# Performance work log

Hardware: AMD Instinct MI355X
Metric: run time of the kernel (lower is better)

## Reference

```python
import jax, jax.numpy as jnp
import numpy as np

B, T, NV, DEG, E = 64, 256, 20000, 8, 128
NSEG, NBUCKET = NV * DEG, 288
F_DIST, F_DIR, F_TT, HID = 50, 50, 50, 100
FEED = 2 * E + F_DIST + F_DIR  # 356


def setup_inputs() -> dict:
    key = jax.random.key(0)
    ks = jax.random.split(key, 32)
    s = 1.0 / np.sqrt(E)
    return {
        "xs_padded": jax.random.randint(ks[0], (B, T), 0, NV),
        "lengths": jax.random.randint(ks[1], (B,), 8, T + 1),
        "xs_actions": jax.random.randint(ks[2], (B, T - 1), 0, DEG),
        "destinations": jax.random.randint(ks[3], (B,), 0, NV),
        "adj_list": jax.random.randint(ks[4], (NV, DEG), 0, NV),
        "seg_ids": jax.random.randint(ks[5], (NV, DEG), 0, NSEG),
        "start_time": 42,
        "locations": jax.random.normal(ks[6], (NV, 2)),
        "time_dist_seg": jax.random.uniform(ks[7], (NSEG, NBUCKET)) * 10.0,
        "emb": jax.random.normal(ks[8], (NV + 2, E)) * 0.01,
        "Wq": jax.random.normal(ks[9], (E, E)) * s,
        "Wk": jax.random.normal(ks[10], (E, E)) * s,
        "Wv": jax.random.normal(ks[11], (E, E)) * s,
        "Wo": jax.random.normal(ks[12], (E, E)) * s,
        "dist_W": jax.random.normal(ks[13], (1, F_DIST)),
        "dist_b": jnp.zeros((F_DIST,)),
        "dir_W": jax.random.normal(ks[14], (2, F_DIR)) * 0.7,
        "dir_b": jnp.zeros((F_DIR,)),
        "tt_W": jax.random.normal(ks[15], (1, F_TT)),
        "tt_b": jnp.zeros((F_TT,)),
        "ob_W1": jax.random.normal(ks[16], (F_TT, F_TT // 2)) * (1.0 / np.sqrt(F_TT)),
        "ob_b1": jnp.zeros((F_TT // 2,)),
        "ob_W2": jax.random.normal(ks[17], (F_TT // 2, 1)) * (1.0 / np.sqrt(F_TT // 2)),
        "ob_b2": jnp.zeros((1,)),
        "om_W1": jax.random.normal(ks[18], (FEED, HID)) * (1.0 / np.sqrt(FEED)),
        "om_b1": jnp.zeros((HID,)),
        "om_W2": jax.random.normal(ks[19], (HID, HID // 2)) * (1.0 / np.sqrt(HID)),
        "om_b2": jnp.zeros((HID // 2,)),
        "om_W3": jax.random.normal(ks[20], (HID // 2, 1)) * (1.0 / np.sqrt(HID // 2)),
        "om_b3": jnp.zeros((1,)),
    }


def reference(xs_padded, lengths, xs_actions, destinations, adj_list, seg_ids,
              start_time, locations, time_dist_seg, emb, Wq, Wk, Wv, Wo,
              dist_W, dist_b, dir_W, dir_b, tt_W, tt_b,
              ob_W1, ob_b1, ob_W2, ob_b2,
              om_W1, om_b1, om_W2, om_b2, om_W3, om_b3):
    # --- embeddings + causal/padding-masked self-attention (flash_att) ---
    x_e = emb[xs_padded]                                       # [B,T,E]
    q, k, v = x_e @ Wq, x_e @ Wk, x_e @ Wv
    scores = jnp.einsum('bqe,bke->bqk', q, k) / jnp.sqrt(jnp.float32(E))
    causal = jnp.triu(jnp.ones((T, T), bool), 1)
    pad = jnp.arange(T)[None, :] >= lengths[:, None]           # key padding [B,T]
    scores = jnp.where(causal[None] | pad[:, None, :], -1e9, scores)
    hidden = jnp.einsum('bqk,bke->bqe', jax.nn.softmax(scores, axis=-1), v) @ Wo

    # --- irregular neighbor gather: route_neighbors only filled for t < len-1 ---
    valid_t = jnp.arange(T)[None, :] < (lengths - 1)[:, None]  # [B,T]
    rn = jnp.where(valid_t[:, :, None], adj_list[xs_padded], 0)  # [B,T,DEG]

    # --- distance to destination feature ---
    dest_c = locations[destinations][:, None, None, :]         # [B,1,1,2]
    nbr_c = locations[rn]                                      # [B,T,DEG,2]
    dist = jnp.abs(nbr_c - dest_c).sum(-1, keepdims=True) * 100.0
    dist_f = dist @ dist_W + dist_b

    # --- direction (unit vector) feature ---
    vec = nbr_c - locations[xs_padded][:, :, None, :]
    unit = vec / (jnp.linalg.norm(vec, axis=-1, keepdims=True) + 1e-8)
    dir_f = unit @ dir_W + dir_b

    # --- travel-time lookup + masked whitening ---
    nmask = rn != 0
    tt = time_dist_seg[seg_ids[xs_padded], start_time]         # [B,T,DEG]
    mf = nmask.astype(tt.dtype)
    cnt = mf.sum()
    mean = (tt * mf).sum() / cnt
    var = (((tt - mean) ** 2) * mf).sum() / (cnt - 1.0)        # unbiased, like torch.std
    tt = (tt - mean) / (jnp.sqrt(var) + 1e-6)
    tt_f = (tt[..., None] @ tt_W + tt_b) * mf[..., None]

    # --- fuse and score neighbors ---
    hid_e = jnp.broadcast_to(hidden[:, :, None, :], (B, T, DEG, E))
    dest_e = jnp.broadcast_to(emb[destinations][:, None, None, :], (B, T, DEG, E))
    feed = jnp.concatenate([hid_e, dist_f, dir_f, dest_e], axis=-1)  # [B,T,DEG,356]

    ob = (jax.nn.relu(tt_f @ ob_W1 + ob_b1) @ ob_W2 + ob_b2).squeeze(-1)
    h1 = jax.nn.relu(feed @ om_W1 + om_b1)
    h2 = jax.nn.relu(h1 @ om_W2 + om_b2)
    logits = (h2 @ om_W3 + om_b3).squeeze(-1) + ob             # [B,T,DEG]

    # --- per-route mean cross-entropy over valid transitions, summed over batch ---
    logp = jax.nn.log_softmax(logits[:, :T - 1], axis=-1)
    nll = -jnp.take_along_axis(logp, xs_actions[..., None], axis=-1).squeeze(-1)
    vmask = (jnp.arange(T - 1)[None, :] < (lengths - 1)[:, None]).astype(nll.dtype)
    per = (nll * vmask).sum(1) / (lengths - 1).astype(nll.dtype)
    return per.sum()
```

## Files before the change

kernel.cpp:

```cpp
#include <hip/hip_runtime.h>
#include <math.h>

#define BB 64
#define TT 256
#define DEG 8
#define EE 128
#define NBUCKET 288
#define HID 100
#define H2 50

constexpr size_t OFF_STATS   = 0;
constexpr size_t OFF_CDIST   = 4;
constexpr size_t OFF_CDIRX   = 104;
constexpr size_t OFF_CDIRY   = 204;
constexpr size_t OFF_BASE    = 304;
constexpr size_t OFF_V25     = 404;
constexpr size_t OFF_C25     = 429;
constexpr size_t OFF_OBZ     = 454;
constexpr size_t OFF_DESTPRE = 456;
constexpr size_t OFF_WF      = 6856;
constexpr size_t OFF_WVF     = 19656;
constexpr size_t OFF_TT      = 32456;
constexpr size_t OFF_Q       = 163528;
constexpr size_t OFF_K       = OFF_Q + 16384 * 128;
constexpr size_t OFF_VP      = OFF_K + 16384 * 128;
constexpr size_t OFF_H1P     = OFF_VP + 16384 * 100;

__global__ void k_prevec(const float* dist_W, const float* dist_b,
                         const float* dir_W, const float* dir_b,
                         const float* tt_W, const float* tt_b,
                         const float* ob_W1, const float* ob_b1,
                         const float* ob_W2, const float* ob_b2,
                         const float* om_W1, const float* om_b1,
                         float* ws, float* out) {
    int j = threadIdx.x;
    if (j < 4) ws[OFF_STATS + j] = 0.f;
    if (j == 0) out[0] = 0.f;
    if (j < HID) {
        float cd = 0.f, cx = 0.f, cy = 0.f, bs = om_b1[j];
        for (int f = 0; f < 50; f++) {
            float w1d = om_W1[(128 + f) * HID + j];
            float w1r = om_W1[(178 + f) * HID + j];
            cd += dist_W[f] * w1d;
            bs += dist_b[f] * w1d + dir_b[f] * w1r;
            cx += dir_W[f] * w1r;
            cy += dir_W[50 + f] * w1r;
        }
        ws[OFF_CDIST + j] = cd; ws[OFF_CDIRX + j] = cx;
        ws[OFF_CDIRY + j] = cy; ws[OFF_BASE + j] = bs;
    }
    if (j < 25) {
        float v = 0.f, c = ob_b1[j];
        for (int i = 0; i < 50; i++) {
            v += tt_W[i] * ob_W1[i * 25 + j];
            c += tt_b[i] * ob_W1[i * 25 + j];
        }
        ws[OFF_V25 + j] = v; ws[OFF_C25 + j] = c;
    }
    if (j == 64) {
        float z = ob_b2[0];
        for (int i = 0; i < 25; i++) z += fmaxf(ob_b1[i], 0.f) * ob_W2[i];
        ws[OFF_OBZ] = z;
    }
}

__global__ void k_destpre(const int* destinations, const float* emb,
                          const float* om_W1, float* ws) {
    __shared__ float er[EE];
    int b = blockIdx.x;
    int d = destinations[b];
    er[threadIdx.x] = emb[(size_t)d * EE + threadIdx.x];
    __syncthreads();
    int m = threadIdx.x;
    if (m < HID) {
        float acc = 0.f;
        for (int i = 0; i < EE; i++) acc += er[i] * om_W1[(228 + i) * HID + m];
        ws[OFF_DESTPRE + b * HID + m] = acc;
    }
}

__global__ void k_wfused(const float* Wo, const float* om_W1, float* ws) {
    __shared__ float wr[EE];
    int i = blockIdx.x;
    wr[threadIdx.x] = Wo[i * EE + threadIdx.x];
    __syncthreads();
    int m = threadIdx.x;
    if (m < HID) {
        float acc = 0.f;
        for (int j = 0; j < EE; j++) acc += wr[j] * om_W1[j * HID + m];
        ws[OFF_WF + i * HID + m] = acc;
    }
}

__global__ void k_wvf(const float* Wv, float* ws) {
    __shared__ float wr[EE];
    int i = blockIdx.x;
    wr[threadIdx.x] = Wv[i * EE + threadIdx.x];
    __syncthreads();
    int m = threadIdx.x;
    if (m < HID) {
        float acc = 0.f;
        const float* WF = ws + OFF_WF;
        for (int j = 0; j < EE; j++) acc += wr[j] * WF[j * HID + m];
        ws[OFF_WVF + i * HID + m] = acc;
    }
}

__global__ void __launch_bounds__(256) k_qkv(const int* xs, const float* emb,
                      const float* Wq, const float* Wk, float* ws) {
    __shared__ float XT[EE][36];
    __shared__ int vids[32];
    int tid = threadIdx.x;
    int r0 = blockIdx.x * 32;
    if (tid < 32) vids[tid] = xs[r0 + tid];
    __syncthreads();
    for (int c = 0; c < 16; c++) {
        int idx = c * 256 + tid;
        int r = idx >> 7, i = idx & 127;
        XT[i][r] = emb[(size_t)vids[r] * EE + i];
    }
    __syncthreads();
    int cg = tid & 31, rg = tid >> 5;
    const float* Wmats[2] = {Wq, Wk};
    float* Omats[2] = {ws + OFF_Q, ws + OFF_K};
    for (int mtx = 0; mtx < 2; mtx++) {
        const float* W = Wmats[mtx];
        float acc[4][4];
        #pragma unroll
        for (int a = 0; a < 4; a++)
            #pragma unroll
            for (int bb = 0; bb < 4; bb++) acc[a][bb] = 0.f;
        #pragma unroll 4
        for (int i = 0; i < EE; i++) {
            float4 av = *(const float4*)&XT[i][rg << 2];
            float4 wv = *(const float4*)&W[i * EE + (cg << 2)];
            acc[0][0] += av.x * wv.x; acc[0][1] += av.x * wv.y; acc[0][2] += av.x * wv.z; acc[0][3] += av.x * wv.w;
            acc[1][0] += av.y * wv.x; acc[1][1] += av.y * wv.y; acc[1][2] += av.y * wv.z; acc[1][3] += av.y * wv.w;
            acc[2][0] += av.z * wv.x; acc[2][1] += av.z * wv.y; acc[2][2] += av.z * wv.z; acc[2][3] += av.z * wv.w;
            acc[3][0] += av.w * wv.x; acc[3][1] += av.w * wv.y; acc[3][2] += av.w * wv.z; acc[3][3] += av.w * wv.w;
        }
        float* O = Omats[mtx];
        #pragma unroll
        for (int j = 0; j < 4; j++)
            *(float4*)&O[(size_t)(r0 + (rg << 2) + j) * EE + (cg << 2)] =
                make_float4(acc[j][0], acc[j][1], acc[j][2], acc[j][3]);
    }
    if (cg < 25) {
        const float* W = ws + OFF_WVF;
        float acc[4][4];
        #pragma unroll
        for (int a = 0; a < 4; a++)
            #pragma unroll
            for (int bb = 0; bb < 4; bb++) acc[a][bb] = 0.f;
        #pragma unroll 4
        for (int i = 0; i < EE; i++) {
            float4 av = *(const float4*)&XT[i][rg << 2];
            float4 wv = *(const float4*)&W[i * HID + (cg << 2)];
            acc[0][0] += av.x * wv.x; acc[0][1] += av.x * wv.y; acc[0][2] += av.x * wv.z; acc[0][3] += av.x * wv.w;
            acc[1][0] += av.y * wv.x; acc[1][1] += av.y * wv.y; acc[1][2] += av.y * wv.z; acc[1][3] += av.y * wv.w;
            acc[2][0] += av.z * wv.x; acc[2][1] += av.z * wv.y; acc[2][2] += av.z * wv.z; acc[2][3] += av.z * wv.w;
            acc[3][0] += av.w * wv.x; acc[3][1] += av.w * wv.y; acc[3][2] += av.w * wv.z; acc[3][3] += av.w * wv.w;
        }
        float* VP = ws + OFF_VP;
        #pragma unroll
        for (int j = 0; j < 4; j++)
            *(float4*)&VP[(size_t)(r0 + (rg << 2) + j) * HID + (cg << 2)] =
                make_float4(acc[j][0], acc[j][1], acc[j][2], acc[j][3]);
    }
}

__global__ void __launch_bounds__(128) k_attn(const int* lengths, float* ws) {
    int blk = blockIdx.x;
    int b = blk >> 8;
    int t = blk & 255;
    int len = lengths[b];
    if (t >= len - 1) return;
    __shared__ float q4s[EE];
    __shared__ float sc[TT];
    __shared__ float redm[2], reds[2];
    int tid = threadIdx.x;
    const float* Q = ws + OFF_Q; const float* K = ws + OFF_K;
    const float* VP = ws + OFF_VP;
    q4s[tid] = Q[(size_t)blk * EE + tid];
    __syncthreads();
    const float4* q4 = (const float4*)q4s;
    float lmax = -1e30f;
    #pragma unroll
    for (int h = 0; h < 2; h++) {
        int kk = tid + h * 128;
        if (kk <= t) {
            const float4* kr = (const float4*)(K + ((size_t)(b * TT + kk)) * EE);
            float s = 0.f;
            #pragma unroll 8
            for (int i = 0; i < EE / 4; i++) {
                float4 a = q4[i]; float4 bb = kr[i];
                s += a.x * bb.x + a.y * bb.y + a.z * bb.z + a.w * bb.w;
            }
            s *= 0.08838834764831845f;
            sc[kk] = s;
            lmax = fmaxf(lmax, s);
        }
    }
    #pragma unroll
    for (int o = 32; o > 0; o >>= 1) lmax = fmaxf(lmax, __shfl_xor(lmax, o, 64));
    if ((tid & 63) == 0) redm[tid >> 6] = lmax;
    __syncthreads();
    float m = fmaxf(redm[0], redm[1]);
    float lsum = 0.f;
    #pragma unroll
    for (int h = 0; h < 2; h++) {
        int kk = tid + h * 128;
        if (kk <= t) { float p = __expf(sc[kk] - m); sc[kk] = p; lsum += p; }
    }
    #pragma unroll
    for (int o = 32; o > 0; o >>= 1) lsum += __shfl_xor(lsum, o, 64);
    if ((tid & 63) == 0) reds[tid >> 6] = lsum;
    __syncthreads();
    float inv = 1.f / (reds[0] + reds[1]);
    if (tid < HID) {
        size_t base = (size_t)(b * TT) * HID + tid;
        float a0 = 0.f, a1 = 0.f, a2 = 0.f, a3 = 0.f;
        int kk = 0;
        for (; kk + 4 <= t + 1; kk += 4) {
            a0 += sc[kk]     * VP[base + (size_t)kk * HID];
            a1 += sc[kk + 1] * VP[base + (size_t)(kk + 1) * HID];
            a2 += sc[kk + 2] * VP[base + (size_t)(kk + 2) * HID];
            a3 += sc[kk + 3] * VP[base + (size_t)(kk + 3) * HID];
        }
        for (; kk <= t; kk++) a0 += sc[kk] * VP[base + (size_t)kk * HID];
        float o = (a0 + a1 + a2 + a3) * inv;
        ws[OFF_H1P + (size_t)blk * HID + tid] =
            o + ws[OFF_BASE + tid] + ws[OFF_DESTPRE + b * HID + tid];
    }
}

__global__ void __launch_bounds__(256) k_stats(const int* xs, const int* lengths, const int* adj,
                        const int* seg, const int* stime, const float* tds,
                        float* ws) {
    int st = *stime;
    float lsum = 0.f, lsq = 0.f, lcnt = 0.f;
    int total = BB * TT * DEG;
    for (int idx = blockIdx.x * blockDim.x + threadIdx.x; idx < total;
         idx += gridDim.x * blockDim.x) {
        int d = idx & 7;
        int bt = idx >> 3;
        int t = bt & 255;
        int b = bt >> 8;
        int len = lengths[b];
        if (t >= len - 1) continue;
        int v = xs[bt];
        int sg = seg[v * DEG + d];
        float tt = tds[(size_t)sg * NBUCKET + st];
        ws[OFF_TT + idx] = tt;
        int a = adj[v * DEG + d];
        if (a != 0) { lsum += tt; lsq += tt * tt; lcnt += 1.f; }
    }
    __shared__ float rs[256], rq[256], rc[256];
    int tid = threadIdx.x;
    rs[tid] = lsum; rq[tid] = lsq; rc[tid] = lcnt;
    __syncthreads();
    for (int s = 128; s > 0; s >>= 1) {
        if (tid < s) { rs[tid] += rs[tid + s]; rq[tid] += rq[tid + s]; rc[tid] += rc[tid + s]; }
        __syncthreads();
    }
    if (tid == 0) {
        atomicAdd(&ws[OFF_STATS + 0], rs[0]);
        atomicAdd(&ws[OFF_STATS + 1], rq[0]);
        atomicAdd(&ws[OFF_STATS + 2], rc[0]);
    }
}

__global__ void __launch_bounds__(256) k_final(
    const int* xs, const int* lengths, const int* xs_actions, const int* destinations,
    const int* adj, const float* locations,
    const float* om_W2, const float* om_b2, const float* om_W3, const float* om_b3,
    const float* ob_W2, const float* ob_b2,
    const float* ws, float* out)
{
    __shared__ float W2T[H2][104];
    __shared__ float h1s[4][DEG][104];
    __shared__ float nlls[4];
    int tid = threadIdx.x;
    for (int idx = tid; idx < HID * H2; idx += 256) {
        int mm = idx / H2, n = idx - mm * H2;
        W2T[n][mm] = om_W2[idx];
    }
    if (tid < 4) nlls[tid] = 0.f;
    int w = tid >> 6, lane = tid & 63;
    int pi = blockIdx.x * 4 + w;
    int b = pi / (TT - 1), t = pi - b * (TT - 1);
    int len = lengths[b];
    bool valid = (t < len - 1);
    int bt = b * TT + t;
    int r = lane >> 3, li = lane & 7;
    __syncthreads();
    float distv = 0.f, uxv = 0.f, uyv = 0.f, obv = 0.f;
    if (valid) {
        float sum = ws[OFF_STATS], sq = ws[OFF_STATS + 1], cnt = ws[OFF_STATS + 2];
        float mean = sum / cnt;
        float var = (sq - cnt * mean * mean) / (cnt - 1.f);
        float sdinv = 1.f / (sqrtf(var) + 1e-6f);
        if (lane < 8) {
            int v = xs[bt];
            int a = adj[v * DEG + lane];
            float nbx = locations[2 * a], nby = locations[2 * a + 1];
            int dst = destinations[b];
            float dxl = locations[2 * dst], dyl = locations[2 * dst + 1];
            float cxl = locations[2 * v], cyl = locations[2 * v + 1];
            distv = (fabsf(nbx - dxl) + fabsf(nby - dyl)) * 100.f;
            float vx = nbx - cxl, vy = nby - cyl;
            float nrm = sqrtf(vx * vx + vy * vy) + 1e-8f;
            uxv = vx / nrm; uyv = vy / nrm;
            float ttn = (ws[OFF_TT + (size_t)bt * 8 + lane] - mean) * sdinv;
            float obp = 0.f;
            for (int j = 0; j < 25; j++)
                obp += fmaxf(ttn * ws[OFF_V25 + j] + ws[OFF_C25 + j], 0.f) * ob_W2[j];
            obv = (a != 0) ? (obp + ob_b2[0]) : ws[OFF_OBZ];
        }
        distv = __shfl(distv, r, 64);
        uxv   = __shfl(uxv, r, 64);
        uyv   = __shfl(uyv, r, 64);
        obv   = __shfl(obv, r, 64);
        const float* H = ws + OFF_H1P + (size_t)bt * HID;
        for (int mm = li; mm < HID; mm += 8) {
            float pre = H[mm] + distv * ws[OFF_CDIST + mm]
                      + uxv * ws[OFF_CDIRX + mm] + uyv * ws[OFF_CDIRY + mm];
            h1s[w][r][mm] = fmaxf(pre, 0.f);
        }
    }
    __syncthreads();
    if (valid) {
        float acc[7] = {0.f, 0.f, 0.f, 0.f, 0.f, 0.f, 0.f};
        const float4* hv4 = (const float4*)h1s[w][r];
        for (int ks = 0; ks < 25; ks++) {
            float4 h = hv4[ks];
            #pragma unroll
            for (int j = 0; j < 7; j++) {
                int n = li + 8 * j;
                if (n < H2) {
                    float4 wv = *(const float4*)&W2T[n][ks << 2];
                    acc[j] += h.x * wv.x + h.y * wv.y + h.z * wv.z + h.w * wv.w;
                }
            }
        }
        float part = 0.f;
        #pragma unroll
        for (int j = 0; j < 7; j++) {
            int n = li + 8 * j;
            if (n < H2) part += fmaxf(acc[j] + om_b2[n], 0.f) * om_W3[n];
        }
        part += __shfl_xor(part, 1, 8);
        part += __shfl_xor(part, 2, 8);
        part += __shfl_xor(part, 4, 8);
        float logit = part + om_b3[0] + obv;
        float lgv[8];
        float mx = -1e30f;
        #pragma unroll
        for (int d = 0; d < 8; d++) {
            lgv[d] = __shfl(logit, d << 3, 64);
            mx = fmaxf(mx, lgv[d]);
        }
        if (lane == 0) {
            int act = xs_actions[b * (TT - 1) + t];
            float se = 0.f, sel = 0.f;
            #pragma unroll
            for (int d = 0; d < 8; d++) {
                se += __expf(lgv[d] - mx);
                if (d == act) sel = lgv[d];
            }
            float nll = mx + __logf(se) - sel;
            nlls[w] = nll / (float)(len - 1);
        }
    }
    __syncthreads();
    if (tid == 0) {
        atomicAdd(out, nlls[0] + nlls[1] + nlls[2] + nlls[3]);
    }
}

extern "C" void kernel_launch(void* const* d_in, const int* in_sizes, int n_in,
                              void* d_out, int out_size, void* d_ws, size_t ws_size,
                              hipStream_t stream) {
    const int* xs_padded    = (const int*)d_in[0];
    const int* lengths      = (const int*)d_in[1];
    const int* xs_actions   = (const int*)d_in[2];
    const int* destinations = (const int*)d_in[3];
    const int* adj_list     = (const int*)d_in[4];
    const int* seg_ids      = (const int*)d_in[5];
    const int* start_time   = (const int*)d_in[6];
    const float* locations  = (const float*)d_in[7];
    const float* tds        = (const float*)d_in[8];
    const float* emb        = (const float*)d_in[9];
    const float* Wq         = (const float*)d_in[10];
    const float* Wk         = (const float*)d_in[11];
    const float* Wv         = (const float*)d_in[12];
    const float* Wo         = (const float*)d_in[13];
    const float* dist_W     = (const float*)d_in[14];
    const float* dist_b     = (const float*)d_in[15];
    const float* dir_W      = (const float*)d_in[16];
    const float* dir_b      = (const float*)d_in[17];
    const float* tt_W       = (const float*)d_in[18];
    const float* tt_b       = (const float*)d_in[19];
    const float* ob_W1      = (const float*)d_in[20];
    const float* ob_b1      = (const float*)d_in[21];
    const float* ob_W2      = (const float*)d_in[22];
    const float* ob_b2      = (const float*)d_in[23];
    const float* om_W1      = (const float*)d_in[24];
    const float* om_b1      = (const float*)d_in[25];
    const float* om_W2      = (const float*)d_in[26];
    const float* om_b2      = (const float*)d_in[27];
    const float* om_W3      = (const float*)d_in[28];
    const float* om_b3      = (const float*)d_in[29];
    float* ws  = (float*)d_ws;
    float* out = (float*)d_out;

    k_prevec<<<1, 128, 0, stream>>>(dist_W, dist_b, dir_W, dir_b, tt_W, tt_b,
                                    ob_W1, ob_b1, ob_W2, ob_b2, om_W1, om_b1, ws, out);
    k_destpre<<<BB, 128, 0, stream>>>(destinations, emb, om_W1, ws);
    k_wfused<<<EE, 128, 0, stream>>>(Wo, om_W1, ws);
    k_wvf<<<EE, 128, 0, stream>>>(Wv, ws);
    k_qkv<<<(BB * TT) / 32, 256, 0, stream>>>(xs_padded, emb, Wq, Wk, ws);
    k_stats<<<256, 256, 0, stream>>>(xs_padded, lengths, adj_list, seg_ids,
                                     start_time, tds, ws);
    k_attn<<<BB * TT, 128, 0, stream>>>(lengths, ws);
    k_final<<<(BB * (TT - 1)) / 4, 256, 0, stream>>>(
        xs_padded, lengths, xs_actions, destinations, adj_list, locations,
        om_W2, om_b2, om_W3, om_b3, ob_W2, ob_b2, ws, out);
}
```

Baseline: 530.5 us.

## Merge setup kernels, fuse QKV with stats, and tile attention over query blocks

Folds the prevec, destination-projection and Wo-fusion kernels into one launch, and runs the QKV projection and the travel-time stats in a single kernel. V is now projected in two steps through shared memory, which removes the separate Wv·WF precompute kernel. Attention processes 16 queries per block and stages K and V tiles in shared memory so they are reused across queries, instead of one block per query. The final kernel handles 16 positions per block to cut block count. This lowers launch count and global K/V traffic, at the cost of more shared memory per block and some wasted work in partially masked tiles.

```diff
diff --git a/kernel.cpp b/kernel.cpp
--- a/kernel.cpp
+++ b/kernel.cpp
@@ -19,254 +19,289 @@
 constexpr size_t OFF_OBZ     = 454;
 constexpr size_t OFF_DESTPRE = 456;
 constexpr size_t OFF_WF      = 6856;
-constexpr size_t OFF_WVF     = 19656;
 constexpr size_t OFF_TT      = 32456;
 constexpr size_t OFF_Q       = 163528;
 constexpr size_t OFF_K       = OFF_Q + 16384 * 128;
 constexpr size_t OFF_VP      = OFF_K + 16384 * 128;
 constexpr size_t OFF_H1P     = OFF_VP + 16384 * 100;
 
-__global__ void k_prevec(const float* dist_W, const float* dist_b,
-                         const float* dir_W, const float* dir_b,
-                         const float* tt_W, const float* tt_b,
-                         const float* ob_W1, const float* ob_b1,
-                         const float* ob_W2, const float* ob_b2,
-                         const float* om_W1, const float* om_b1,
-                         float* ws, float* out) {
+__global__ void __launch_bounds__(256) k_setup(
+    const int* destinations, const float* emb, const float* Wo,
+    const float* dist_W, const float* dist_b, const float* dir_W, const float* dir_b,
+    const float* tt_W, const float* tt_b, const float* ob_W1, const float* ob_b1,
+    const float* ob_W2, const float* ob_b2, const float* om_W1, const float* om_b1,
+    float* ws, float* out) {
+    __shared__ float sh[EE];
+    int blk = blockIdx.x;
     int j = threadIdx.x;
-    if (j < 4) ws[OFF_STATS + j] = 0.f;
-    if (j == 0) out[0] = 0.f;
-    if (j < HID) {
-        float cd = 0.f, cx = 0.f, cy = 0.f, bs = om_b1[j];
-        for (int f = 0; f < 50; f++) {
-            float w1d = om_W1[(128 + f) * HID + j];
-            float w1r = om_W1[(178 + f) * HID + j];
-            cd += dist_W[f] * w1d;
-            bs += dist_b[f] * w1d + dir_b[f] * w1r;
-            cx += dir_W[f] * w1r;
-            cy += dir_W[50 + f] * w1r;
-        }
-        ws[OFF_CDIST + j] = cd; ws[OFF_CDIRX + j] = cx;
-        ws[OFF_CDIRY + j] = cy; ws[OFF_BASE + j] = bs;
-    }
-    if (j < 25) {
-        float v = 0.f, c = ob_b1[j];
-        for (int i = 0; i < 50; i++) {
-            v += tt_W[i] * ob_W1[i * 25 + j];
-            c += tt_b[i] * ob_W1[i * 25 + j];
-        }
-        ws[OFF_V25 + j] = v; ws[OFF_C25 + j] = c;
-    }
-    if (j == 64) {
-        float z = ob_b2[0];
-        for (int i = 0; i < 25; i++) z += fmaxf(ob_b1[i], 0.f) * ob_W2[i];
-        ws[OFF_OBZ] = z;
+    if (blk == 0) {
+        if (j < 4) ws[OFF_STATS + j] = 0.f;
+        if (j == 0) out[0] = 0.f;
+        if (j < HID) {
+            float cd = 0.f, cx = 0.f, cy = 0.f, bs = om_b1[j];
+            for (int f = 0; f < 50; f++) {
+                float w1d = om_W1[(128 + f) * HID + j];
+                float w1r = om_W1[(178 + f) * HID + j];
+                cd += dist_W[f] * w1d;
+                bs += dist_b[f] * w1d + dir_b[f] * w1r;
+                cx += dir_W[f] * w1r;
+                cy += dir_W[50 + f] * w1r;
+            }
+            ws[OFF_CDIST + j] = cd; ws[OFF_CDIRX + j] = cx;
+            ws[OFF_CDIRY + j] = cy; ws[OFF_BASE + j] = bs;
+        }
+        if (j >= 128 && j < 153) {
+            int jj = j - 128;
+            float v = 0.f, c = ob_b1[jj];
+            for (int i = 0; i < 50; i++) {
+                v += tt_W[i] * ob_W1[i * 25 + jj];
+                c += tt_b[i] * ob_W1[i * 25 + jj];
+            }
+            ws[OFF_V25 + jj] = v; ws[OFF_C25 + jj] = c;
+        }
+        if (j == 200) {
+            float z = ob_b2[0];
+            for (int i = 0; i < 25; i++) z += fmaxf(ob_b1[i], 0.f) * ob_W2[i];
+            ws[OFF_OBZ] = z;
+        }
+    } else if (blk <= 64) {
+        int b = blk - 1;
+        if (j < EE) sh[j] = emb[(size_t)destinations[b] * EE + j];
+        __syncthreads();
+        if (j < HID) {
+            float acc = 0.f;
+            for (int i = 0; i < EE; i++) acc += sh[i] * om_W1[(228 + i) * HID + j];
+            ws[OFF_DESTPRE + b * HID + j] = acc;
+        }
+    } else {
+        int i = blk - 65;
+        if (j < EE) sh[j] = Wo[i * EE + j];
+        __syncthreads();
+        if (j < HID) {
+            float acc = 0.f;
+            for (int jj = 0; jj < EE; jj++) acc += sh[jj] * om_W1[jj * HID + j];
+            ws[OFF_WF + i * HID + j] = acc;
+        }
     }
 }
 
-__global__ void k_destpre(const int* destinations, const float* emb,
-                          const float* om_W1, float* ws) {
-    __shared__ float er[EE];
-    int b = blockIdx.x;
-    int d = destinations[b];
-    er[threadIdx.x] = emb[(size_t)d * EE + threadIdx.x];
-    __syncthreads();
-    int m = threadIdx.x;
-    if (m < HID) {
-        float acc = 0.f;
-        for (int i = 0; i < EE; i++) acc += er[i] * om_W1[(228 + i) * HID + m];
-        ws[OFF_DESTPRE + b * HID + m] = acc;
+__global__ void __launch_bounds__(256) k_mid(
+    const int* xs, const int* lengths, const int* adj, const int* seg,
+    const int* stime, const float* tds, const float* emb,
+    const float* Wq, const float* Wk, const float* Wv, float* ws) {
+    __shared__ float smem[2 * 128 * 36 + 32];
+    int blk = blockIdx.x;
+    int tid = threadIdx.x;
+    if (blk < 512) {
+        float (*XT)[36]  = (float(*)[36])smem;
+        float (*T1T)[36] = (float(*)[36])(smem + 128 * 36);
+        int* vids = (int*)(smem + 2 * 128 * 36);
+        int r0 = blk * 32;
+        if (tid < 32) vids[tid] = xs[r0 + tid];
+        __syncthreads();
+        for (int c = 0; c < 16; c++) {
+            int idx = c * 256 + tid;
+            int r = idx >> 7, i = idx & 127;
+            XT[i][r] = emb[(size_t)vids[r] * EE + i];
+        }
+        __syncthreads();
+        int cg = tid & 31, rg = tid >> 5;
+        const float* Wmats[2] = {Wq, Wk};
+        float* Omats[2] = {ws + OFF_Q, ws + OFF_K};
+        for (int mtx = 0; mtx < 2; mtx++) {
+            const float* W = Wmats[mtx];
+            float acc[4][4];
+            #pragma unroll
+            for (int a = 0; a < 4; a++)
+                #pragma unroll
+                for (int bb = 0; bb < 4; bb++) acc[a][bb] = 0.f;
+            #pragma unroll 4
+            for (int i = 0; i < EE; i++) {
+                float4 av = *(const float4*)&XT[i][rg << 2];
+                float4 wv = *(const float4*)&W[i * EE + (cg << 2)];
+                acc[0][0] += av.x * wv.x; acc[0][1] += av.x * wv.y; acc[0][2] += av.x * wv.z; acc[0][3] += av.x * wv.w;
+                acc[1][0] += av.y * wv.x; acc[1][1] += av.y * wv.y; acc[1][2] += av.y * wv.z; acc[1][3] += av.y * wv.w;
+                acc[2][0] += av.z * wv.x; acc[2][1] += av.z * wv.y; acc[2][2] += av.z * wv.z; acc[2][3] += av.z * wv.w;
+                acc[3][0] += av.w * wv.x; acc[3][1] += av.w * wv.y; acc[3][2] += av.w * wv.z; acc[3][3] += av.w * wv.w;
+            }
+            float* O = Omats[mtx];
+            #pragma unroll
+            for (int jj = 0; jj < 4; jj++)
+                *(float4*)&O[(size_t)(r0 + (rg << 2) + jj) * EE + (cg << 2)] =
+                    make_float4(acc[jj][0], acc[jj][1], acc[jj][2], acc[jj][3]);
+        }
+        {
+            float acc[4][4];
+            #pragma unroll
+            for (int a = 0; a < 4; a++)
+                #pragma unroll
+                for (int bb = 0; bb < 4; bb++) acc[a][bb] = 0.f;
+            #pragma unroll 4
+            for (int i = 0; i < EE; i++) {
+                float4 av = *(const float4*)&XT[i][rg << 2];
+                float4 wv = *(const float4*)&Wv[i * EE + (cg << 2)];
+                acc[0][0] += av.x * wv.x; acc[0][1] += av.x * wv.y; acc[0][2] += av.x * wv.z; acc[0][3] += av.x * wv.w;
+                acc[1][0] += av.y * wv.x; acc[1][1] += av.y * wv.y; acc[1][2] += av.y * wv.z; acc[1][3] += av.y * wv.w;
+                acc[2][0] += av.z * wv.x; acc[2][1] += av.z * wv.y; acc[2][2] += av.z * wv.z; acc[2][3] += av.z * wv.w;
+                acc[3][0] += av.w * wv.x; acc[3][1] += av.w * wv.y; acc[3][2] += av.w * wv.z; acc[3][3] += av.w * wv.w;
+            }
+            #pragma unroll
+            for (int jj = 0; jj < 4; jj++)
+                #pragma unroll
+                for (int ii = 0; ii < 4; ii++)
+                    T1T[(cg << 2) + ii][(rg << 2) + jj] = acc[jj][ii];
+        }
+        __syncthreads();
+        if (cg < 25) {
+            const float* WF = ws + OFF_WF;
+            float acc[4][4];
+            #pragma unroll
+            for (int a = 0; a < 4; a++)
+                #pragma unroll
+                for (int bb = 0; bb < 4; bb++) acc[a][bb] = 0.f;
+            #pragma unroll 4
+            for (int i = 0; i < EE; i++) {
+                float4 av = *(const float4*)&T1T[i][rg << 2];
+                float4 wv = *(const float4*)&WF[i * HID + (cg << 2)];
+                acc[0][0] += av.x * wv.x; acc[0][1] += av.x * wv.y; acc[0][2] += av.x * wv.z; acc[0][3] += av.x * wv.w;
+                acc[1][0] += av.y * wv.x; acc[1][1] += av.y * wv.y; acc[1][2] += av.y * wv.z; acc[1][3] += av.y * wv.w;
+                acc[2][0] += av.z * wv.x; acc[2][1] += av.z * wv.y; acc[2][2] += av.z * wv.z; acc[2][3] += av.z * wv.w;
+                acc[3][0] += av.w * wv.x; acc[3][1] += av.w * wv.y; acc[3][2] += av.w * wv.z; acc[3][3] += av.w * wv.w;
+            }
+            float* VP = ws + OFF_VP;
+            #pragma unroll
+            for (int jj = 0; jj < 4; jj++)
+                *(float4*)&VP[(size_t)(r0 + (rg << 2) + jj) * HID + (cg << 2)] =
+                    make_float4(acc[jj][0], acc[jj][1], acc[jj][2], acc[jj][3]);
+        }
+    } else {
+        float* rs = smem; float* rq = smem + 256; float* rc = smem + 512;
+        int st = *stime;
+        float lsum = 0.f, lsq = 0.f, lcnt = 0.f;
+        int total = BB * TT * DEG;
+        for (int idx = (blk - 512) * 256 + tid; idx < total; idx += 256 * 256) {
+            int d = idx & 7;
+            int bt = idx >> 3;
+            int t = bt & 255;
+            int b = bt >> 8;
+            int len = lengths[b];
+            if (t >= len - 1) continue;
+            int v = xs[bt];
+            int sg = seg[v * DEG + d];
+            float tt = tds[(size_t)sg * NBUCKET + st];
+            ws[OFF_TT + idx] = tt;
+            int a = adj[v * DEG + d];
+            if (a != 0) { lsum += tt; lsq += tt * tt; lcnt += 1.f; }
+        }
+        rs[tid] = lsum; rq[tid] = lsq; rc[tid] = lcnt;
+        __syncthreads();
+        for (int s = 128; s > 0; s >>= 1) {
+            if (tid < s) { rs[tid] += rs[tid + s]; rq[tid] += rq[tid + s]; rc[tid] += rc[tid + s]; }
+            __syncthreads();
+        }
+        if (tid == 0) {
+            atomicAdd(&ws[OFF_STATS + 0], rs[0]);
+            atomicAdd(&ws[OFF_STATS + 1], rq[0]);
+            atomicAdd(&ws[OFF_STATS + 2], rc[0]);
+        }
     }
 }
 
-__global__ void k_wfused(const float* Wo, const float* om_W1, float* ws) {
-    __shared__ float wr[EE];
-    int i = blockIdx.x;
-    wr[threadIdx.x] = Wo[i * EE + threadIdx.x];
-    __syncthreads();
-    int m = threadIdx.x;
-    if (m < HID) {
-        float acc = 0.f;
-        for (int j = 0; j < EE; j++) acc += wr[j] * om_W1[j * HID + m];
-        ws[OFF_WF + i * HID + m] = acc;
-    }
-}
-
-__global__ void k_wvf(const float* Wv, float* ws) {
-    __shared__ float wr[EE];
-    int i = blockIdx.x;
-    wr[threadIdx.x] = Wv[i * EE + threadIdx.x];
-    __syncthreads();
-    int m = threadIdx.x;
-    if (m < HID) {
-        float acc = 0.f;
-        const float* WF = ws + OFF_WF;
-        for (int j = 0; j < EE; j++) acc += wr[j] * WF[j * HID + m];
-        ws[OFF_WVF + i * HID + m] = acc;
-    }
-}
-
-__global__ void __launch_bounds__(256) k_qkv(const int* xs, const float* emb,
-                      const float* Wq, const float* Wk, float* ws) {
-    __shared__ float XT[EE][36];
-    __shared__ int vids[32];
+__global__ void __launch_bounds__(256) k_attn(const int* lengths, float* ws) {
+    int b = blockIdx.x >> 4;
+    int tile = blockIdx.x & 15;
+    int t0 = tile << 4;
+    int len = lengths[b];
+    if (t0 >= len - 1) return;
+    int nk = t0 + 16;
+    int nm = nk >> 4;
+    __shared__ float Qs[16][132];
+    __shared__ float S[16][260];
+    __shared__ float KV[32 * 136];
     int tid = threadIdx.x;
-    int r0 = blockIdx.x * 32;
-    if (tid < 32) vids[tid] = xs[r0 + tid];
-    __syncthreads();
-    for (int c = 0; c < 16; c++) {
-        int idx = c * 256 + tid;
-        int r = idx >> 7, i = idx & 127;
-        XT[i][r] = emb[(size_t)vids[r] * EE + i];
-    }
-    __syncthreads();
-    int cg = tid & 31, rg = tid >> 5;
-    const float* Wmats[2] = {Wq, Wk};
-    float* Omats[2] = {ws + OFF_Q, ws + OFF_K};
-    for (int mtx = 0; mtx < 2; mtx++) {
-        const float* W = Wmats[mtx];
-        float acc[4][4];
+    const float* Q  = ws + OFF_Q;
+    const float* K  = ws + OFF_K;
+    const float* VP = ws + OFF_VP;
+    {
+        const float* Qg = Q + ((size_t)(b * TT + t0)) * EE;
+        for (int idx = tid; idx < 512; idx += 256) {
+            int r = idx >> 5, c4 = (idx & 31) << 2;
+            *(float4*)&Qs[r][c4] = *(const float4*)&Qg[r * EE + c4];
+        }
+    }
+    int q = tid >> 4, li = tid & 15;
+    int tq = t0 + q;
+    float sreg[16];
+    #pragma unroll
+    for (int m = 0; m < 16; m++) sreg[m] = -1e30f;
+    float (*Ks)[136] = (float(*)[136])KV;
+    int ktend = ((nk + 31) >> 5) << 5;
+    for (int kt = 0; kt < ktend; kt += 32) {
+        __syncthreads();
+        const float* Kg = K + ((size_t)(b * TT + kt)) * EE;
+        for (int idx = tid; idx < 1024; idx += 256) {
+            int r = idx >> 5, c4 = (idx & 31) << 2;
+            *(float4*)&Ks[r][c4] = *(const float4*)&Kg[r * EE + c4];
+        }
+        __syncthreads();
+        int k0 = kt + li, k1 = kt + li + 16;
+        float s0 = 0.f, s1 = 0.f;
+        const float4* q4  = (const float4*)Qs[q];
+        const float4* k4a = (const float4*)Ks[li];
+        const float4* k4b = (const float4*)Ks[li + 16];
+        #pragma unroll 8
+        for (int i = 0; i < 32; i++) {
+            float4 a = q4[i];
+            float4 x = k4a[i];
+            float4 y = k4b[i];
+            s0 += a.x * x.x + a.y * x.y + a.z * x.z + a.w * x.w;
+            s1 += a.x * y.x + a.y * y.y + a.z * y.z + a.w * y.w;
+        }
+        int m0 = kt >> 4;
+        if (k0 < nk && k0 <= tq) sreg[m0]     = s0 * 0.08838834764831845f;
+        if (k1 < nk && k1 <= tq) sreg[m0 + 1] = s1 * 0.08838834764831845f;
+    }
+    float mx = -1e30f;
+    for (int m = 0; m < nm; m++) mx = fmaxf(mx, sreg[m]);
+    #pragma unroll
+    for (int o = 1; o < 16; o <<= 1) mx = fmaxf(mx, __shfl_xor(mx, o, 16));
+    float lsum = 0.f;
+    for (int m = 0; m < nm; m++) { float p = __expf(sreg[m] - mx); sreg[m] = p; lsum += p; }
+    #pragma unroll
+    for (int o = 1; o < 16; o <<= 1) lsum += __shfl_xor(lsum, o, 16);
+    float inv = 1.f / lsum;
+    for (int m = 0; m < nm; m++) S[q][li + (m << 4)] = sreg[m];
+    float acc[7];
+    #pragma unroll
+    for (int j = 0; j < 7; j++) acc[j] = 0.f;
+    float (*Vs)[104] = (float(*)[104])KV;
+    for (int vt = 0; vt < nk; vt += 32) {
+        __syncthreads();
+        const float* Vg = VP + ((size_t)(b * TT + vt)) * HID;
+        for (int idx = tid; idx < 800; idx += 256) {
+            int r = idx / 25, c4 = (idx - r * 25) << 2;
+            *(float4*)&Vs[r][c4] = *(const float4*)&Vg[r * HID + c4];
+        }
+        __syncthreads();
+        int kmax = nk - vt; if (kmax > 32) kmax = 32;
+        for (int k = 0; k < kmax; k++) {
+            float p = S[q][vt + k];
+            #pragma unroll
+            for (int j = 0; j < 7; j++) {
+                int c = li + (j << 4);
+                if (c < HID) acc[j] += p * Vs[k][c];
+            }
+        }
+    }
+    if (tq < len - 1) {
+        float* H = ws + OFF_H1P + (size_t)(b * TT + tq) * HID;
+        const float* BASEv = ws + OFF_BASE;
+        const float* DP = ws + OFF_DESTPRE + b * HID;
         #pragma unroll
-        for (int a = 0; a < 4; a++)
-            #pragma unroll
-            for (int bb = 0; bb < 4; bb++) acc[a][bb] = 0.f;
-        #pragma unroll 4
-        for (int i = 0; i < EE; i++) {
-            float4 av = *(const float4*)&XT[i][rg << 2];
-            float4 wv = *(const float4*)&W[i * EE + (cg << 2)];
-            acc[0][0] += av.x * wv.x; acc[0][1] += av.x * wv.y; acc[0][2] += av.x * wv.z; acc[0][3] += av.x * wv.w;
-            acc[1][0] += av.y * wv.x; acc[1][1] += av.y * wv.y; acc[1][2] += av.y * wv.z; acc[1][3] += av.y * wv.w;
-            acc[2][0] += av.z * wv.x; acc[2][1] += av.z * wv.y; acc[2][2] += av.z * wv.z; acc[2][3] += av.z * wv.w;
-            acc[3][0] += av.w * wv.x; acc[3][1] += av.w * wv.y; acc[3][2] += av.w * wv.z; acc[3][3] += av.w * wv.w;
-        }
-        float* O = Omats[mtx];
-        #pragma unroll
-        for (int j = 0; j < 4; j++)
-            *(float4*)&O[(size_t)(r0 + (rg << 2) + j) * EE + (cg << 2)] =
-                make_float4(acc[j][0], acc[j][1], acc[j][2], acc[j][3]);
-    }
-    if (cg < 25) {
-        const float* W = ws + OFF_WVF;
-        float acc[4][4];
-        #pragma unroll
-        for (int a = 0; a < 4; a++)
-            #pragma unroll
-            for (int bb = 0; bb < 4; bb++) acc[a][bb] = 0.f;
-        #pragma unroll 4
-        for (int i = 0; i < EE; i++) {
-            float4 av = *(const float4*)&XT[i][rg << 2];
-            float4 wv = *(const float4*)&W[i * HID + (cg << 2)];
-            acc[0][0] += av.x * wv.x; acc[0][1] += av.x * wv.y; acc[0][2] += av.x * wv.z; acc[0][3] += av.x * wv.w;
-            acc[1][0] += av.y * wv.x; acc[1][1] += av.y * wv.y; acc[1][2] += av.y * wv.z; acc[1][3] += av.y * wv.w;
-            acc[2][0] += av.z * wv.x; acc[2][1] += av.z * wv.y; acc[2][2] += av.z * wv.z; acc[2][3] += av.z * wv.w;
-            acc[3][0] += av.w * wv.x; acc[3][1] += av.w * wv.y; acc[3][2] += av.w * wv.z; acc[3][3] += av.w * wv.w;
-        }
-        float* VP = ws + OFF_VP;
-        #pragma unroll
-        for (int j = 0; j < 4; j++)
-            *(float4*)&VP[(size_t)(r0 + (rg << 2) + j) * HID + (cg << 2)] =
-                make_float4(acc[j][0], acc[j][1], acc[j][2], acc[j][3]);
-    }
-}
-
-__global__ void __launch_bounds__(128) k_attn(const int* lengths, float* ws) {
-    int blk = blockIdx.x;
-    int b = blk >> 8;
-    int t = blk & 255;
-    int len = lengths[b];
-    if (t >= len - 1) return;
-    __shared__ float q4s[EE];
-    __shared__ float sc[TT];
-    __shared__ float redm[2], reds[2];
-    int tid = threadIdx.x;
-    const float* Q = ws + OFF_Q; const float* K = ws + OFF_K;
-    const float* VP = ws + OFF_VP;
-    q4s[tid] = Q[(size_t)blk * EE + tid];
-    __syncthreads();
-    const float4* q4 = (const float4*)q4s;
-    float lmax = -1e30f;
-    #pragma unroll
-    for (int h = 0; h < 2; h++) {
-        int kk = tid + h * 128;
-        if (kk <= t) {
-            const float4* kr = (const float4*)(K + ((size_t)(b * TT + kk)) * EE);
-            float s = 0.f;
-            #pragma unroll 8
-            for (int i = 0; i < EE / 4; i++) {
-                float4 a = q4[i]; float4 bb = kr[i];
-                s += a.x * bb.x + a.y * bb.y + a.z * bb.z + a.w * bb.w;
-            }
-            s *= 0.08838834764831845f;
-            sc[kk] = s;
-            lmax = fmaxf(lmax, s);
-        }
-    }
-    #pragma unroll
-    for (int o = 32; o > 0; o >>= 1) lmax = fmaxf(lmax, __shfl_xor(lmax, o, 64));
-    if ((tid & 63) == 0) redm[tid >> 6] = lmax;
-    __syncthreads();
-    float m = fmaxf(redm[0], redm[1]);
-    float lsum = 0.f;
-    #pragma unroll
-    for (int h = 0; h < 2; h++) {
-        int kk = tid + h * 128;
-        if (kk <= t) { float p = __expf(sc[kk] - m); sc[kk] = p; lsum += p; }
-    }
-    #pragma unroll
-    for (int o = 32; o > 0; o >>= 1) lsum += __shfl_xor(lsum, o, 64);
-    if ((tid & 63) == 0) reds[tid >> 6] = lsum;
-    __syncthreads();
-    float inv = 1.f / (reds[0] + reds[1]);
-    if (tid < HID) {
-        size_t base = (size_t)(b * TT) * HID + tid;
-        float a0 = 0.f, a1 = 0.f, a2 = 0.f, a3 = 0.f;
-        int kk = 0;
-        for (; kk + 4 <= t + 1; kk += 4) {
-            a0 += sc[kk]     * VP[base + (size_t)kk * HID];
-            a1 += sc[kk + 1] * VP[base + (size_t)(kk + 1) * HID];
-            a2 += sc[kk + 2] * VP[base + (size_t)(kk + 2) * HID];
-            a3 += sc[kk + 3] * VP[base + (size_t)(kk + 3) * HID];
-        }
-        for (; kk <= t; kk++) a0 += sc[kk] * VP[base + (size_t)kk * HID];
-        float o = (a0 + a1 + a2 + a3) * inv;
-        ws[OFF_H1P + (size_t)blk * HID + tid] =
-            o + ws[OFF_BASE + tid] + ws[OFF_DESTPRE + b * HID + tid];
-    }
-}
-
-__global__ void __launch_bounds__(256) k_stats(const int* xs, const int* lengths, const int* adj,
-                        const int* seg, const int* stime, const float* tds,
-                        float* ws) {
-    int st = *stime;
-    float lsum = 0.f, lsq = 0.f, lcnt = 0.f;
-    int total = BB * TT * DEG;
-    for (int idx = blockIdx.x * blockDim.x + threadIdx.x; idx < total;
-         idx += gridDim.x * blockDim.x) {
-        int d = idx & 7;
-        int bt = idx >> 3;
-        int t = bt & 255;
-        int b = bt >> 8;
-        int len = lengths[b];
-        if (t >= len - 1) continue;
-        int v = xs[bt];
-        int sg = seg[v * DEG + d];
-        float tt = tds[(size_t)sg * NBUCKET + st];
-        ws[OFF_TT + idx] = tt;
-        int a = adj[v * DEG + d];
-        if (a != 0) { lsum += tt; lsq += tt * tt; lcnt += 1.f; }
-    }
-    __shared__ float rs[256], rq[256], rc[256];
-    int tid = threadIdx.x;
-    rs[tid] = lsum; rq[tid] = lsq; rc[tid] = lcnt;
-    __syncthreads();
-    for (int s = 128; s > 0; s >>= 1) {
-        if (tid < s) { rs[tid] += rs[tid + s]; rq[tid] += rq[tid + s]; rc[tid] += rc[tid + s]; }
-        __syncthreads();
-    }
-    if (tid == 0) {
-        atomicAdd(&ws[OFF_STATS + 0], rs[0]);
-        atomicAdd(&ws[OFF_STATS + 1], rq[0]);
-        atomicAdd(&ws[OFF_STATS + 2], rc[0]);
+        for (int j = 0; j < 7; j++) {
+            int c = li + (j << 4);
+            if (c < HID) H[c] = acc[j] * inv + BASEv[c] + DP[c];
+        }
     }
 }
 
@@ -287,89 +322,88 @@
     }
     if (tid < 4) nlls[tid] = 0.f;
     int w = tid >> 6, lane = tid & 63;
-    int pi = blockIdx.x * 4 + w;
-    int b = pi / (TT - 1), t = pi - b * (TT - 1);
-    int len = lengths[b];
-    bool valid = (t < len - 1);
-    int bt = b * TT + t;
     int r = lane >> 3, li = lane & 7;
+    float sum = ws[OFF_STATS], sq = ws[OFF_STATS + 1], cnt = ws[OFF_STATS + 2];
+    float mean = sum / cnt;
+    float var = (sq - cnt * mean * mean) / (cnt - 1.f);
+    float sdinv = 1.f / (sqrtf(var) + 1e-6f);
     __syncthreads();
-    float distv = 0.f, uxv = 0.f, uyv = 0.f, obv = 0.f;
-    if (valid) {
-        float sum = ws[OFF_STATS], sq = ws[OFF_STATS + 1], cnt = ws[OFF_STATS + 2];
-        float mean = sum / cnt;
-        float var = (sq - cnt * mean * mean) / (cnt - 1.f);
-        float sdinv = 1.f / (sqrtf(var) + 1e-6f);
-        if (lane < 8) {
-            int v = xs[bt];
-            int a = adj[v * DEG + lane];
-            float nbx = locations[2 * a], nby = locations[2 * a + 1];
-            int dst = destinations[b];
-            float dxl = locations[2 * dst], dyl = locations[2 * dst + 1];
-            float cxl = locations[2 * v], cyl = locations[2 * v + 1];
-            distv = (fabsf(nbx - dxl) + fabsf(nby - dyl)) * 100.f;
-            float vx = nbx - cxl, vy = nby - cyl;
-            float nrm = sqrtf(vx * vx + vy * vy) + 1e-8f;
-            uxv = vx / nrm; uyv = vy / nrm;
-            float ttn = (ws[OFF_TT + (size_t)bt * 8 + lane] - mean) * sdinv;
-            float obp = 0.f;
-            for (int j = 0; j < 25; j++)
-                obp += fmaxf(ttn * ws[OFF_V25 + j] + ws[OFF_C25 + j], 0.f) * ob_W2[j];
-            obv = (a != 0) ? (obp + ob_b2[0]) : ws[OFF_OBZ];
-        }
-        distv = __shfl(distv, r, 64);
-        uxv   = __shfl(uxv, r, 64);
-        uyv   = __shfl(uyv, r, 64);
-        obv   = __shfl(obv, r, 64);
-        const float* H = ws + OFF_H1P + (size_t)bt * HID;
-        for (int mm = li; mm < HID; mm += 8) {
-            float pre = H[mm] + distv * ws[OFF_CDIST + mm]
-                      + uxv * ws[OFF_CDIRX + mm] + uyv * ws[OFF_CDIRY + mm];
-            h1s[w][r][mm] = fmaxf(pre, 0.f);
-        }
-    }
-    __syncthreads();
-    if (valid) {
-        float acc[7] = {0.f, 0.f, 0.f, 0.f, 0.f, 0.f, 0.f};
-        const float4* hv4 = (const float4*)h1s[w][r];
-        for (int ks = 0; ks < 25; ks++) {
-            float4 h = hv4[ks];
+    for (int it = 0; it < 4; it++) {
+        int pi = blockIdx.x * 16 + it * 4 + w;
+        int b = pi / (TT - 1), t = pi - b * (TT - 1);
+        int len = lengths[b];
+        bool valid = (t < len - 1);
+        int bt = b * TT + t;
+        if (valid) {
+            float distv = 0.f, uxv = 0.f, uyv = 0.f, obv = 0.f;
+            if (lane < 8) {
+                int v = xs[bt];
+                int a = adj[v * DEG + lane];
+                float nbx = locations[2 * a], nby = locations[2 * a + 1];
+                int dst = destinations[b];
+                float dxl = locations[2 * dst], dyl = locations[2 * dst + 1];
+                float cxl = locations[2 * v], cyl = locations[2 * v + 1];
+                distv = (fabsf(nbx - dxl) + fabsf(nby - dyl)) * 100.f;
+                float vx = nbx - cxl, vy = nby - cyl;
+                float nrm = sqrtf(vx * vx + vy * vy) + 1e-8f;
+                uxv = vx / nrm; uyv = vy / nrm;
+                float ttn = (ws[OFF_TT + (size_t)bt * 8 + lane] - mean) * sdinv;
+                float obp = 0.f;
+                for (int j = 0; j < 25; j++)
+                    obp += fmaxf(ttn * ws[OFF_V25 + j] + ws[OFF_C25 + j], 0.f) * ob_W2[j];
+                obv = (a != 0) ? (obp + ob_b2[0]) : ws[OFF_OBZ];
+            }
+            distv = __shfl(distv, r, 64);
+            uxv   = __shfl(uxv, r, 64);
+            uyv   = __shfl(uyv, r, 64);
+            obv   = __shfl(obv, r, 64);
+            const float* H = ws + OFF_H1P + (size_t)bt * HID;
+            for (int mm = li; mm < HID; mm += 8) {
+                float pre = H[mm] + distv * ws[OFF_CDIST + mm]
+                          + uxv * ws[OFF_CDIRX + mm] + uyv * ws[OFF_CDIRY + mm];
+                h1s[w][r][mm] = fmaxf(pre, 0.f);
+            }
+            float acc[7] = {0.f, 0.f, 0.f, 0.f, 0.f, 0.f, 0.f};
+            const float4* hv4 = (const float4*)h1s[w][r];
+            for (int ks = 0; ks < 25; ks++) {
+                float4 h = hv4[ks];
+                #pragma unroll
+                for (int j = 0; j < 7; j++) {
+                    int n = li + 8 * j;
+                    if (n < H2) {
+                        float4 wv = *(const float4*)&W2T[n][ks << 2];
+                        acc[j] += h.x * wv.x + h.y * wv.y + h.z * wv.z + h.w * wv.w;
+                    }
+                }
+            }
+            float part = 0.f;
             #pragma unroll
             for (int j = 0; j < 7; j++) {
                 int n = li + 8 * j;
-                if (n < H2) {
-                    float4 wv = *(const float4*)&W2T[n][ks << 2];
-                    acc[j] += h.x * wv.x + h.y * wv.y + h.z * wv.z + h.w * wv.w;
+                if (n < H2) part += fmaxf(acc[j] + om_b2[n], 0.f) * om_W3[n];
+            }
+            part += __shfl_xor(part, 1, 8);
+            part += __shfl_xor(part, 2, 8);
+            part += __shfl_xor(part, 4, 8);
+            float logit = part + om_b3[0] + obv;
+            float lgv[8];
+            float mx = -1e30f;
+            #pragma unroll
+            for (int d = 0; d < 8; d++) {
+                lgv[d] = __shfl(logit, d << 3, 64);
+                mx = fmaxf(mx, lgv[d]);
+            }
+            if (lane == 0) {
+                int act = xs_actions[b * (TT - 1) + t];
+                float se = 0.f, sel = 0.f;
+                #pragma unroll
+                for (int d = 0; d < 8; d++) {
+                    se += __expf(lgv[d] - mx);
+                    if (d == act) sel = lgv[d];
                 }
-            }
-        }
-        float part = 0.f;
-        #pragma unroll
-        for (int j = 0; j < 7; j++) {
-            int n = li + 8 * j;
-            if (n < H2) part += fmaxf(acc[j] + om_b2[n], 0.f) * om_W3[n];
-        }
-        part += __shfl_xor(part, 1, 8);
-        part += __shfl_xor(part, 2, 8);
-        part += __shfl_xor(part, 4, 8);
-        float logit = part + om_b3[0] + obv;
-        float lgv[8];
-        float mx = -1e30f;
-        #pragma unroll
-        for (int d = 0; d < 8; d++) {
-            lgv[d] = __shfl(logit, d << 3, 64);
-            mx = fmaxf(mx, lgv[d]);
-        }
-        if (lane == 0) {
-            int act = xs_actions[b * (TT - 1) + t];
-            float se = 0.f, sel = 0.f;
-            #pragma unroll
-            for (int d = 0; d < 8; d++) {
-                se += __expf(lgv[d] - mx);
-                if (d == act) sel = lgv[d];
-            }
-            float nll = mx + __logf(se) - sel;
-            nlls[w] = nll / (float)(len - 1);
+                float nll = mx + __logf(se) - sel;
+                nlls[w] += nll / (float)(len - 1);
+            }
         }
     }
     __syncthreads();
@@ -414,16 +448,13 @@
     float* ws  = (float*)d_ws;
     float* out = (float*)d_out;
 
-    k_prevec<<<1, 128, 0, stream>>>(dist_W, dist_b, dir_W, dir_b, tt_W, tt_b,
-                                    ob_W1, ob_b1, ob_W2, ob_b2, om_W1, om_b1, ws, out);
-    k_destpre<<<BB, 128, 0, stream>>>(destinations, emb, om_W1, ws);
-    k_wfused<<<EE, 128, 0, stream>>>(Wo, om_W1, ws);
-    k_wvf<<<EE, 128, 0, stream>>>(Wv, ws);
-    k_qkv<<<(BB * TT) / 32, 256, 0, stream>>>(xs_padded, emb, Wq, Wk, ws);
-    k_stats<<<256, 256, 0, stream>>>(xs_padded, lengths, adj_list, seg_ids,
-                                     start_time, tds, ws);
-    k_attn<<<BB * TT, 128, 0, stream>>>(lengths, ws);
-    k_final<<<(BB * (TT - 1)) / 4, 256, 0, stream>>>(
+    k_setup<<<193, 256, 0, stream>>>(destinations, emb, Wo, dist_W, dist_b,
+                                     dir_W, dir_b, tt_W, tt_b, ob_W1, ob_b1,
+                                     ob_W2, ob_b2, om_W1, om_b1, ws, out);
+    k_mid<<<768, 256, 0, stream>>>(xs_padded, lengths, adj_list, seg_ids,
+                                   start_time, tds, emb, Wq, Wk, Wv, ws);
+    k_attn<<<BB * 16, 256, 0, stream>>>(lengths, ws);
+    k_final<<<1020, 256, 0, stream>>>(
         xs_padded, lengths, xs_actions, destinations, adj_list, locations,
         om_W2, om_b2, om_W3, om_b3, ob_W2, ob_b2, ws, out);
 }
```

Result: faster. 483.9 us (-8.8%).
